# Optimization experiments

Hardware: AMD Instinct MI355X
Metric: run time of the kernel (lower is better)

The kernel has to match this reference:

```python
import jax, jax.numpy as jnp
import numpy as np

# dims (Nemotron-H 8B class mamba mixer)
HID = 4096      # hidden_size
NH = 128        # mamba_num_heads
HD = 64         # mamba_head_dim
DIN = NH * HD   # intermediate_size = 8192
G = 8           # n_groups
N = 128         # ssm_state_size
K = 4           # conv_kernel
CS = 256        # chunk_size
EPS = 1e-5
GROUP_SIZE = DIN // G
CONV_DIM = DIN + 2 * G * N           # 10240
PROJ = DIN + CONV_DIM + NH           # 18560 = gate | xBC | dt


def segment_sum(x):
    """x: [..., k] -> [..., k, k]; out[i,j] = sum_{m=j+1..i} x[m], -inf above diag."""
    k = x.shape[-1]
    xe = jnp.broadcast_to(x[..., None], x.shape + (k,))
    xe = jnp.where(jnp.tril(jnp.ones((k, k), bool), -1), xe, 0.0)
    s = jnp.cumsum(xe, axis=-2)
    return jnp.where(jnp.tril(jnp.ones((k, k), bool), 0), s, -jnp.inf)


def setup_inputs() -> dict:
    key = jax.random.key(0)
    ks = jax.random.split(key, 9)
    std = 0.02
    return {
        "hidden_states": jax.random.normal(ks[0], (2, 2048, HID), jnp.float32),
        "in_proj_w": jax.random.normal(ks[1], (PROJ, HID), jnp.float32) * std,
        "conv_w": jax.random.normal(ks[2], (CONV_DIM, 1, K), jnp.float32) * 0.1,
        "conv_b": jax.random.normal(ks[3], (CONV_DIM,), jnp.float32) * 0.01,
        "dt_bias": jax.random.uniform(ks[4], (NH,), jnp.float32, -4.0, -2.0),
        "A_log": jnp.log(jax.random.uniform(ks[5], (NH,), jnp.float32, 1.0, 16.0)),
        "D": jnp.ones((NH,), jnp.float32),
        "norm_w": jnp.ones((DIN,), jnp.float32),
        "out_proj_w": jax.random.normal(ks[8], (HID, DIN), jnp.float32) * std,
    }


def reference(hidden_states, in_proj_w, conv_w, conv_b, dt_bias, A_log, D, norm_w, out_proj_w):
    b, l, _ = hidden_states.shape
    zxbcdt = hidden_states @ in_proj_w.T                       # [b,l,PROJ]
    gate = zxbcdt[..., :DIN]
    xBC = zxbcdt[..., DIN:DIN + CONV_DIM]
    dt = zxbcdt[..., DIN + CONV_DIM:]                          # [b,l,NH]

    # causal depthwise conv1d + silu
    conv = jax.lax.conv_general_dilated(
        jnp.transpose(xBC, (0, 2, 1)), conv_w, (1,), [(K - 1, 0)],
        feature_group_count=CONV_DIM, dimension_numbers=("NCH", "OIH", "NCH"))
    xBC = jax.nn.silu(jnp.transpose(conv + conv_b[None, :, None], (0, 2, 1)))

    x = xBC[..., :DIN].reshape(b, l, NH, HD)
    B = xBC[..., DIN:DIN + G * N].reshape(b, l, G, N)
    C = xBC[..., DIN + G * N:].reshape(b, l, G, N)
    B = jnp.repeat(B, NH // G, axis=2)                         # [b,l,NH,N]
    C = jnp.repeat(C, NH // G, axis=2)

    A = -jnp.exp(A_log)                                        # [NH]
    dt = jax.nn.softplus(dt + dt_bias)                         # [b,l,NH]; limit (0,inf) is a no-op

    pad = (CS - l % CS) % CS
    def padl(t):
        return jnp.pad(t, [(0, 0), (0, pad)] + [(0, 0)] * (t.ndim - 2))

    D_res = D[None, None, :, None] * padl(x)                   # [b,L,NH,HD]
    xs = x * dt[..., None]
    Adt = A[None, None, :] * dt                                # [b,l,NH]

    nc = (l + pad) // CS
    def chunk(t):
        return padl(t).reshape((b, nc, CS) + t.shape[2:])
    xs, B, C = chunk(xs), chunk(B), chunk(C)                   # [b,c,k,h,*]
    Ac = jnp.transpose(chunk(Adt), (0, 3, 1, 2))               # [b,h,c,k]
    A_cumsum = jnp.cumsum(Ac, axis=-1)

    # 1. intra-chunk (diagonal blocks)
    L = jnp.exp(segment_sum(Ac))                               # [b,h,c,k,k]
    Gm = jnp.einsum("bcihn,bcjhn->bhcij", C, B)
    Y_diag = jnp.einsum("bhcij,bcjhd->bcihd", Gm * L, xs)

    # 2. chunk states
    decay_states = jnp.exp(A_cumsum[..., -1:] - A_cumsum)      # [b,h,c,k]
    states = jnp.einsum("bckhn,bhck,bckhd->bchdn", B, decay_states, xs)

    # 3. inter-chunk recurrence
    A_tail = jnp.pad(A_cumsum[..., -1], ((0, 0), (0, 0), (1, 0)))
    decay_chunk = jnp.exp(segment_sum(A_tail))                 # [b,h,c+1,c+1]
    states = jnp.concatenate([jnp.zeros_like(states[:, :1]), states], axis=1)
    new_states = jnp.einsum("bhzc,bchdn->bzhdn", decay_chunk, states)
    states = new_states[:, :-1]                                # [b,c,h,d,n]

    # 4. state -> output
    state_decay = jnp.exp(A_cumsum)                            # [b,h,c,k]
    Y_off = jnp.einsum("bckhn,bchdn,bhck->bckhd", C, states, state_decay)

    y = (Y_diag + Y_off).reshape(b, l + pad, NH, HD) + D_res
    y = y[:, :l].reshape(b, l, DIN)

    # gated grouped RMSNorm
    y = y * jax.nn.silu(gate)
    yg = y.reshape(b, l, G, GROUP_SIZE)
    var = jnp.mean(yg * yg, axis=-1, keepdims=True)
    y = (yg * jax.lax.rsqrt(var + EPS)).reshape(b, l, DIN) * norm_w
    return y @ out_proj_w.T
```

## Files before the change

### kernel.cpp

```cpp
#include <hip/hip_runtime.h>
#include <hip/hip_bf16.h>
#include <math.h>

#define HID 4096
#define NH 128
#define HD 64
#define DIN 8192
#define G 8
#define NSTATE 128
#define CS 256
#define GROUP_SIZE 1024
#define CONV_DIM 10240
#define ZXW 18432
#define BATCH 2
#define SEQ 2048
#define NT (BATCH*SEQ)
#define NC 8
#define DTSK 16

typedef __attribute__((ext_vector_type(8))) short bf16x8;
typedef __attribute__((ext_vector_type(4))) float f32x4;
typedef __attribute__((ext_vector_type(8))) unsigned short u16x8;
typedef __attribute__((ext_vector_type(4))) unsigned short u16x4;

__device__ __forceinline__ float sigmoidf_(float x){ return 1.f/(1.f+expf(-x)); }
__device__ __forceinline__ float siluf_(float x){ return x*sigmoidf_(x); }
__device__ __forceinline__ float softplusf_(float x){ return (x>20.f)? x : log1pf(expf(x)); }
__device__ __forceinline__ float b2f(unsigned short u){ union{unsigned int i; float f;} x; x.i = ((unsigned int)u)<<16; return x.f; }
__device__ __forceinline__ unsigned short f2b(float f){ __hip_bfloat16 h = __float2bfloat16(f); return *(unsigned short*)&h; }

__device__ __forceinline__ void gload_lds16(const void* g, void* l) {
  __builtin_amdgcn_global_load_lds((const __attribute__((address_space(1))) unsigned int*)g,
                                   (__attribute__((address_space(3))) unsigned int*)l, 16, 0, 0);
}
__device__ __forceinline__ bf16x8 ld8bf(const __hip_bfloat16* p){ return *(const bf16x8*)p; }

__device__ __forceinline__ void cast8(const float* in, __hip_bfloat16* out) {
  const float4* p = (const float4*)in;
  float4 a = p[0], b = p[1];
  union { __hip_bfloat16 h[8]; int4 v; } o;
  o.h[0]=__float2bfloat16(a.x); o.h[1]=__float2bfloat16(a.y);
  o.h[2]=__float2bfloat16(a.z); o.h[3]=__float2bfloat16(a.w);
  o.h[4]=__float2bfloat16(b.x); o.h[5]=__float2bfloat16(b.y);
  o.h[6]=__float2bfloat16(b.z); o.h[7]=__float2bfloat16(b.w);
  *(int4*)out = o.v;
}

__global__ __launch_bounds__(256)
void cast3_kernel(const float* __restrict__ hs, __hip_bfloat16* __restrict__ hs_bf,
                  const float* __restrict__ w_in, __hip_bfloat16* __restrict__ w_in_bf,
                  const float* __restrict__ w_out, __hip_bfloat16* __restrict__ w_out_bf) {
  const size_t n0 = (size_t)NT*HID/8;
  const size_t n1 = (size_t)ZXW*HID/8;
  const size_t n2 = (size_t)HID*DIN/8;
  const size_t ntot = n0 + n1 + n2;
  size_t i = (size_t)blockIdx.x * 256 + threadIdx.x;
  size_t stride = (size_t)gridDim.x * 256;
  for (; i < ntot; i += stride) {
    if (i < n0)            cast8(hs   + i*8,        hs_bf   + i*8);
    else if (i < n0 + n1)  cast8(w_in + (i-n0)*8,   w_in_bf + (i-n0)*8);
    else                   cast8(w_out+ (i-n0-n1)*8, w_out_bf+ (i-n0-n1)*8);
  }
}

template<bool OUT_BF16>
__global__ __launch_bounds__(512)
void gemm_bf16_256(const __hip_bfloat16* __restrict__ A, const __hip_bfloat16* __restrict__ B,
                   void* __restrict__ Cout, int M, int N, int K) {
  const int nMt = M >> 8, nNt = N >> 8;
  const int nwg = nMt * nNt;
  const int cpx = nwg >> 3;
  const int lin = blockIdx.x;
  const int swz = (lin & 7) * cpx + (lin >> 3);
  const int mt = swz % nMt, ntile = swz / nMt;
  const int rowBase = mt << 8;
  const int colBase = ntile << 8;

  __shared__ short As[4][8192];
  __shared__ short Bs[4][8192];

  const int tid = threadIdx.x;
  const int lane = tid & 63, wid = tid >> 6;
  const int wr = wid >> 2, wc = wid & 3;
  const int l15 = lane & 15, l4 = lane >> 4;

  const int r0 = tid >> 2,        c0 = (tid & 3) ^ ((r0 >> 1) & 3);
  const int r1 = (512+tid) >> 2,  c1 = ((512+tid) & 3) ^ ((r1 >> 1) & 3);
  const __hip_bfloat16* gA0 = A + (size_t)(rowBase + r0)*K + c0*8;
  const __hip_bfloat16* gA1 = A + (size_t)(rowBase + r1)*K + c1*8;
  const __hip_bfloat16* gB0 = B + (size_t)(colBase + r0)*K + c0*8;
  const __hip_bfloat16* gB1 = B + (size_t)(colBase + r1)*K + c1*8;
  const int ld0 = wid*512, ld1 = 4096 + wid*512;

#define STAGE_A(q, kt) do { \
    gload_lds16(gA0 + (size_t)(kt)*32, (void*)&As[q][ld0]); \
    gload_lds16(gA1 + (size_t)(kt)*32, (void*)&As[q][ld1]); \
  } while(0)
#define STAGE_B(q, kt) do { \
    gload_lds16(gB0 + (size_t)(kt)*32, (void*)&Bs[q][ld0]); \
    gload_lds16(gB1 + (size_t)(kt)*32, (void*)&Bs[q][ld1]); \
  } while(0)

  int aoff[8], boff[4];
  #pragma unroll
  for (int m=0;m<8;++m){ int r = wr*128 + m*16 + l15; aoff[m] = r*32 + ((l4 ^ ((r>>1)&3))*8); }
  #pragma unroll
  for (int n=0;n<4;++n){ int r = wc*64  + n*16 + l15; boff[n] = r*32 + ((l4 ^ ((r>>1)&3))*8); }

  f32x4 acc[8][4] = {};
  const int NKT = K >> 5;

  STAGE_A(0,0); STAGE_B(0,0);
  STAGE_A(1,1); STAGE_B(1,1);
  STAGE_A(2,2); STAGE_B(2,2);
  asm volatile("s_waitcnt vmcnt(8)" ::: "memory");
  __builtin_amdgcn_s_barrier();

  for (int t = 0; t < NKT; ++t) {
    const short* ab = &As[t&3][0];
    const short* bb = &Bs[t&3][0];
    const int q3 = (t+3)&3;
    bf16x8 a[4], b[4], a2[4];
    #pragma unroll
    for (int m=0;m<4;++m) a[m] = *(const bf16x8*)&ab[aoff[m]];
    #pragma unroll
    for (int n=0;n<4;++n) b[n] = *(const bf16x8*)&bb[boff[n]];
    if (t + 3 < NKT) STAGE_A(q3, t+3);
    __builtin_amdgcn_s_barrier();
    asm volatile("s_waitcnt lgkmcnt(0)" ::: "memory");
    __builtin_amdgcn_sched_barrier(0);
    __builtin_amdgcn_s_setprio(1);
    #pragma unroll
    for (int m=0;m<4;++m)
      #pragma unroll
      for (int n=0;n<4;++n)
        acc[m][n] = __builtin_amdgcn_mfma_f32_16x16x32_bf16(a[m], b[n], acc[m][n], 0, 0, 0);
    __builtin_amdgcn_s_setprio(0);
    __builtin_amdgcn_s_barrier();
    #pragma unroll
    for (int m=0;m<4;++m) a2[m] = *(const bf16x8*)&ab[aoff[m+4]];
    if (t + 3 < NKT) STAGE_B(q3, t+3);
    const int rem = NKT - 1 - t;
    if (rem >= 3)      asm volatile("s_waitcnt vmcnt(8)" ::: "memory");
    else if (rem == 2) asm volatile("s_waitcnt vmcnt(4)" ::: "memory");
    else if (rem == 1) asm volatile("s_waitcnt vmcnt(0)" ::: "memory");
    __builtin_amdgcn_s_barrier();
    asm volatile("s_waitcnt lgkmcnt(0)" ::: "memory");
    __builtin_amdgcn_sched_barrier(0);
    __builtin_amdgcn_s_setprio(1);
    #pragma unroll
    for (int m=0;m<4;++m)
      #pragma unroll
      for (int n=0;n<4;++n)
        acc[m+4][n] = __builtin_amdgcn_mfma_f32_16x16x32_bf16(a2[m], b[n], acc[m+4][n], 0, 0, 0);
    __builtin_amdgcn_s_setprio(0);
    __builtin_amdgcn_s_barrier();
  }
#undef STAGE_A
#undef STAGE_B

  #pragma unroll
  for (int m=0;m<8;++m) {
    int row0 = rowBase + wr*128 + m*16 + l4*4;
    #pragma unroll
    for (int n=0;n<4;++n) {
      int col = colBase + wc*64 + n*16 + l15;
      #pragma unroll
      for (int j=0;j<4;++j) {
        if (OUT_BF16)
          ((__hip_bfloat16*)Cout)[(size_t)(row0+j)*N + col] = __float2bfloat16(acc[m][n][j]);
        else
          ((float*)Cout)[(size_t)(row0+j)*N + col] = acc[m][n][j];
      }
    }
  }
}

__global__ __launch_bounds__(256)
void dt_gemm_splitk(const float* __restrict__ A, const float* __restrict__ B,
                    float* __restrict__ partial) {
  __shared__ float As[16][132];
  __shared__ float Bs[16][132];
  const int tid = threadIdx.x;
  const int tx = tid & 15, ty = tid >> 4;
  const int rowBase = blockIdx.y * 128;
  const int k0 = blockIdx.x * (HID/DTSK);
  float acc[8][8] = {};
  for (int kt = k0; kt < k0 + HID/DTSK; kt += 16) {
    for (int e = tid; e < 128*16; e += 256) {
      int r = e >> 4, c = e & 15;
      As[c][r] = A[(size_t)(rowBase + r) * HID + kt + c];
      Bs[c][r] = B[(size_t)r * HID + kt + c];
    }
    __syncthreads();
    #pragma unroll
    for (int kk = 0; kk < 16; ++kk) {
      float a[8], bv[8];
      #pragma unroll
      for (int i = 0; i < 8; ++i) a[i] = As[kk][ty*8+i];
      #pragma unroll
      for (int j = 0; j < 8; ++j) bv[j] = Bs[kk][tx*8+j];
      #pragma unroll
      for (int i = 0; i < 8; ++i)
        #pragma unroll
        for (int j = 0; j < 8; ++j)
          acc[i][j] += a[i]*bv[j];
    }
    __syncthreads();
  }
  float* outp = partial + (size_t)blockIdx.x * NT * NH;
  for (int i = 0; i < 8; ++i) {
    size_t ro = (size_t)(rowBase + ty*8 + i) * NH + tx*8;
    #pragma unroll
    for (int j = 0; j < 8; ++j) outp[ro + j] = acc[i][j];
  }
}

__global__ __launch_bounds__(256)
void dt_scan_kernel(const float* __restrict__ partial, const float* __restrict__ dt_bias,
                    const float* __restrict__ A_log, float* __restrict__ dt_sp,
                    float* __restrict__ Acs) {
  int bid = blockIdx.x;
  int c = bid % NC;
  int h = (bid / NC) % NH;
  int b = bid / (NC*NH);
  int k = threadIdx.x;
  int t = b*SEQ + c*CS + k;
  float raw = dt_bias[h];
  #pragma unroll
  for (int sk = 0; sk < DTSK; ++sk) raw += partial[(size_t)sk*NT*NH + (size_t)t*NH + h];
  float dtv = softplusf_(raw);
  dt_sp[(size_t)t*NH + h] = dtv;
  float adt = -expf(A_log[h]) * dtv;
  __shared__ float s[CS];
  s[k] = adt;
  __syncthreads();
  for (int off = 1; off < CS; off <<= 1) {
    float v = (k >= off) ? s[k-off] : 0.f;
    __syncthreads();
    s[k] += v;
    __syncthreads();
  }
  Acs[((size_t)(b*NH + h)*NC + c)*CS + k] = s[k];
}

__global__ __launch_bounds__(256)
void conv_fused_kernel(const __hip_bfloat16* __restrict__ zx, const float* __restrict__ w,
                       const float* __restrict__ bias,
                       const float* __restrict__ dt_sp, const float* __restrict__ Acs,
                       __hip_bfloat16* __restrict__ xsT, __hip_bfloat16* __restrict__ xwT,
                       __hip_bfloat16* __restrict__ Bbf, __hip_bfloat16* __restrict__ Cbf,
                       __hip_bfloat16* __restrict__ BT) {
  const int tt = blockIdx.x;
  const int ct = blockIdx.y;
  const int t0 = tt*64;
  const int ch0 = ct*64;
  const int tid = threadIdx.x;
  __shared__ unsigned short T[64][72];
  __shared__ float dts[64], ews[64];

  const bool isX = (ch0 < DIN);
  const bool isB = (ch0 >= DIN) && (ch0 < DIN + G*NSTATE);

  if (isX && tid < 64) {
    int h = ch0 >> 6;
    int t = t0 + tid;
    dts[tid] = dt_sp[(size_t)t*NH + h];
    int b = t0 >> 11, cc = (t0 >> 8) & 7, k0 = t0 & 255;
    const float* acs = Acs + ((size_t)(b*NH+h)*NC + cc)*CS;
    ews[tid] = __expf(acs[CS-1] - acs[k0 + tid]);
  }

  const int l0 = t0 & (SEQ-1);
  #pragma unroll
  for (int it = 0; it < 2; ++it) {
    int r = tid >> 2;
    int c8 = (tid & 3) + it*4;
    int cb = ch0 + c8*8;
    float acc[8];
    *(float4*)&acc[0] = *(const float4*)&bias[cb];
    *(float4*)&acc[4] = *(const float4*)&bias[cb+4];
    float4 wv[8];
    #pragma unroll
    for (int q=0;q<8;++q) wv[q] = *(const float4*)&w[(cb+q)*4];
    #pragma unroll
    for (int k=0;k<4;++k) {
      if (l0 + r - 3 + k >= 0) {
        u16x8 v = *(const u16x8*)&zx[(size_t)(t0+r-3+k)*ZXW + DIN + cb];
        #pragma unroll
        for (int q=0;q<8;++q) acc[q] += b2f(v[q]) * ((const float*)&wv[q])[k];
      }
    }
    u16x8 o;
    #pragma unroll
    for (int q=0;q<8;++q) o[q] = f2b(siluf_(acc[q]));
    if (isX || isB) {
      #pragma unroll
      for (int q=0;q<8;++q) T[c8*8+q][r] = o[q];
    }
    if (!isX) {
      if (isB) *(u16x8*)&Bbf[(size_t)(t0+r)*(G*NSTATE) + (cb - DIN)] = o;
      else     *(u16x8*)&Cbf[(size_t)(t0+r)*(G*NSTATE) + (cb - DIN - G*NSTATE)] = o;
    }
  }
  if (!isX && !isB) return;
  __syncthreads();
  #pragma unroll
  for (int it = 0; it < 2; ++it) {
    int ch = tid >> 2;
    int tc = (tid & 3) + it*4;
    u16x8 v = *(const u16x8*)&T[ch][tc*8];
    if (isX) {
      u16x8 a, wv2;
      #pragma unroll
      for (int q=0;q<8;++q) {
        float f = b2f(v[q]);
        float fs = f * dts[tc*8+q];
        a[q]   = f2b(fs);
        wv2[q] = f2b(fs * ews[tc*8+q]);
      }
      *(u16x8*)&xsT[(size_t)(ch0+ch)*NT + t0 + tc*8] = a;
      *(u16x8*)&xwT[(size_t)(ch0+ch)*NT + t0 + tc*8] = wv2;
    } else {
      *(u16x8*)&BT[(size_t)(ch0 - DIN + ch)*NT + t0 + tc*8] = v;
    }
  }
}

__global__ __launch_bounds__(256)
void chunk_states_mfma(const __hip_bfloat16* __restrict__ xwT, const __hip_bfloat16* __restrict__ BT,
                       float* __restrict__ states) {
  int h = blockIdx.x, bc = blockIdx.y;
  int g = h >> 4;
  int b = bc >> 3, c = bc & 7;
  int tbase = b*SEQ + c*CS;
  int tid = threadIdx.x, lane = tid & 63, w = tid >> 6;
  int l15 = lane & 15, l4 = lane >> 4;
  int n0 = w*32;
  const __hip_bfloat16* xp = xwT + (size_t)(h*64 + l15)*NT + tbase + l4*8;
  const __hip_bfloat16* bp = BT + (size_t)(g*128 + n0 + l15)*NT + tbase + l4*8;
  f32x4 acc[4][2] = {};
  for (int kc = 0; kc < 8; ++kc) {
    bf16x8 xf[4], bf2[2];
    #pragma unroll
    for (int tm=0;tm<4;++tm) xf[tm] = ld8bf(xp + (size_t)(tm*16)*NT + kc*32);
    #pragma unroll
    for (int tn=0;tn<2;++tn) bf2[tn] = ld8bf(bp + (size_t)(tn*16)*NT + kc*32);
    #pragma unroll
    for (int tm=0;tm<4;++tm)
      #pragma unroll
      for (int tn=0;tn<2;++tn)
        acc[tm][tn] = __builtin_amdgcn_mfma_f32_16x16x32_bf16(xf[tm], bf2[tn], acc[tm][tn], 0, 0, 0);
  }
  float* out = states + ((size_t)bc*NH + h)*(HD*NSTATE);
  #pragma unroll
  for (int tm=0;tm<4;++tm)
    #pragma unroll
    for (int tn=0;tn<2;++tn)
      #pragma unroll
      for (int q=0;q<4;++q)
        out[(size_t)(tm*16 + l4*4 + q)*NSTATE + n0 + tn*16 + l15] = acc[tm][tn][q];
}

__global__ void state_recurrence_kernel(const float* __restrict__ states, const float* __restrict__ Acs,
                                        __hip_bfloat16* __restrict__ states_bf) {
  int idx = blockIdx.x*256 + threadIdx.x;
  int dn = idx & 8191;
  int h = (idx >> 13) & 127;
  int b = idx >> 20;
  float S = 0.f;
  for (int c = 0; c < NC; ++c) {
    size_t off = ((size_t)(b*NC + c)*NH + h)*8192 + dn;
    float v = states[off];
    states_bf[off] = __float2bfloat16(S);
    float decay = expf(Acs[((size_t)(b*NH+h)*NC + c)*CS + CS-1]);
    S = S*decay + v;
  }
}

__global__ __launch_bounds__(256)
void y_mfma_kernel(const __hip_bfloat16* __restrict__ zx,
                   const __hip_bfloat16* __restrict__ Cn,
                   const __hip_bfloat16* __restrict__ Bn,
                   const __hip_bfloat16* __restrict__ xsT,
                   const __hip_bfloat16* __restrict__ Sbf,
                   const float* __restrict__ dt_sp,
                   const float* __restrict__ Acs,
                   const float* __restrict__ Dp,
                   __hip_bfloat16* __restrict__ ybf) {
  int h = blockIdx.x;
  int bc = blockIdx.y;
  int c = bc & 7, b = bc >> 3;
  int g = h >> 4;
  int tbase = b*SEQ + c*CS;
  int tid = threadIdx.x, lane = tid & 63, w = tid >> 6;
  int l15 = lane & 15, l4 = lane >> 4;
  int i0 = w*64;
  __shared__ float acs_s[CS];
  __shared__ unsigned short P[4][64][72];
  acs_s[tid] = Acs[((size_t)(b*NH+h)*NC + c)*CS + tid];
  __syncthreads();

  float acs_i[4], rd[4];
  float Dh = Dp[h];
  #pragma unroll
  for (int ti=0;ti<4;++ti) {
    int ig = i0 + ti*16 + l15;
    acs_i[ti] = acs_s[ig];
    rd[ti] = Dh / dt_sp[(size_t)(tbase+ig)*NH + h];
  }
  const __hip_bfloat16* Cbase = Cn + (size_t)tbase*1024 + g*128;
  const __hip_bfloat16* Bbase = Bn + (size_t)tbase*1024 + g*128;
  const __hip_bfloat16* xbase = xsT + (size_t)(h*64 + l15)*NT + tbase;

  f32x4 accY[4][4] = {};
  for (int jb = 0; jb <= w; ++jb) {
    int j0 = jb*64;
    f32x4 sacc[4][4] = {};
    for (int kc = 0; kc < 4; ++kc) {
      bf16x8 bfr[4], cfr[4];
      #pragma unroll
      for (int tj=0;tj<4;++tj) bfr[tj] = ld8bf(Bbase + (size_t)(j0 + tj*16 + l15)*1024 + kc*32 + l4*8);
      #pragma unroll
      for (int ti=0;ti<4;++ti) cfr[ti] = ld8bf(Cbase + (size_t)(i0 + ti*16 + l15)*1024 + kc*32 + l4*8);
      #pragma unroll
      for (int tj=0;tj<4;++tj)
        #pragma unroll
        for (int ti=0;ti<4;++ti)
          sacc[tj][ti] = __builtin_amdgcn_mfma_f32_16x16x32_bf16(bfr[tj], cfr[ti], sacc[tj][ti], 0, 0, 0);
    }
    #pragma unroll
    for (int tj=0;tj<4;++tj)
      #pragma unroll
      for (int ti=0;ti<4;++ti) {
        int ig = i0 + ti*16 + l15;
        float ai = acs_i[ti];
        u16x4 pk;
        #pragma unroll
        for (int q=0;q<4;++q) {
          int jg = j0 + tj*16 + l4*4 + q;
          float v = (jg <= ig) ? sacc[tj][ti][q] * __expf(ai - acs_s[jg]) : 0.f;
          if (jg == ig) v += rd[ti];
          pk[q] = f2b(v);
        }
        *(u16x4*)&P[w][ti*16 + l15][tj*16 + l4*4] = pk;
      }
    #pragma unroll
    for (int kc2 = 0; kc2 < 2; ++kc2) {
      bf16x8 xf[4], pf[4];
      #pragma unroll
      for (int tm=0;tm<4;++tm) xf[tm] = ld8bf(xbase + (size_t)(tm*16)*NT + j0 + kc2*32 + l4*8);
      #pragma unroll
      for (int ti=0;ti<4;++ti) pf[ti] = *(const bf16x8*)&P[w][ti*16 + l15][kc2*32 + l4*8];
      #pragma unroll
      for (int tm=0;tm<4;++tm)
        #pragma unroll
        for (int ti=0;ti<4;++ti)
          accY[tm][ti] = __builtin_amdgcn_mfma_f32_16x16x32_bf16(xf[tm], pf[ti], accY[tm][ti], 0, 0, 0);
    }
  }
  const __hip_bfloat16* Sb = Sbf + ((size_t)bc*NH + h)*(HD*NSTATE);
  f32x4 oacc[4][4] = {};
  for (int kc = 0; kc < 4; ++kc) {
    bf16x8 sf[4], cfr[4];
    #pragma unroll
    for (int tm=0;tm<4;++tm) sf[tm] = ld8bf(Sb + (size_t)(tm*16 + l15)*NSTATE + kc*32 + l4*8);
    #pragma unroll
    for (int ti=0;ti<4;++ti) cfr[ti] = ld8bf(Cbase + (size_t)(i0 + ti*16 + l15)*1024 + kc*32 + l4*8);
    #pragma unroll
    for (int tm=0;tm<4;++tm)
      #pragma unroll
      for (int ti=0;ti<4;++ti)
        oacc[tm][ti] = __builtin_amdgcn_mfma_f32_16x16x32_bf16(sf[tm], cfr[ti], oacc[tm][ti], 0, 0, 0);
  }
  #pragma unroll
  for (int ti=0;ti<4;++ti) {
    int ig = i0 + ti*16 + l15;
    int t = tbase + ig;
    float sd = __expf(acs_i[ti]);
    #pragma unroll
    for (int tm=0;tm<4;++tm) {
      int ch0 = h*64 + tm*16 + l4*4;
      u16x4 gv = *(const u16x4*)&zx[(size_t)t*ZXW + ch0];
      u16x4 out;
      #pragma unroll
      for (int q=0;q<4;++q) {
        float yv = accY[tm][ti][q] + sd * oacc[tm][ti][q];
        yv *= siluf_(b2f(gv[q]));
        out[q] = f2b(yv);
      }
      *(u16x4*)&ybf[(size_t)t*DIN + ch0] = out;
    }
  }
}

__global__ __launch_bounds__(256)
void groupnorm_bf16_kernel(unsigned short* __restrict__ y, const float* __restrict__ norm_w) {
  int bid = blockIdx.x;
  int g = bid % G;
  int t = bid / G;
  unsigned short* yp = y + (size_t)t*DIN + g*GROUP_SIZE;
  int tid = threadIdx.x;
  u16x4 v = *(const u16x4*)&yp[tid*4];
  float f[4]; float ss = 0.f;
  #pragma unroll
  for (int j=0;j<4;++j) { f[j] = b2f(v[j]); ss += f[j]*f[j]; }
  #pragma unroll
  for (int off = 32; off > 0; off >>= 1) ss += __shfl_xor(ss, off);
  __shared__ float wsum[4];
  int wave = tid >> 6;
  if ((tid & 63) == 0) wsum[wave] = ss;
  __syncthreads();
  float tot = wsum[0]+wsum[1]+wsum[2]+wsum[3];
  float rs = rsqrtf(tot/(float)GROUP_SIZE + 1e-5f);
  const float* nw = norm_w + g*GROUP_SIZE + tid*4;
  u16x4 o;
  #pragma unroll
  for (int j=0;j<4;++j) o[j] = f2b(f[j] * rs * nw[j]);
  *(u16x4*)&yp[tid*4] = o;
}

extern "C" void kernel_launch(void* const* d_in, const int* in_sizes, int n_in,
                              void* d_out, int out_size, void* d_ws, size_t ws_size,
                              hipStream_t stream) {
  const float* hs        = (const float*)d_in[0];
  const float* in_proj_w = (const float*)d_in[1];
  const float* conv_w    = (const float*)d_in[2];
  const float* conv_b    = (const float*)d_in[3];
  const float* dt_bias   = (const float*)d_in[4];
  const float* A_log     = (const float*)d_in[5];
  const float* Dp        = (const float*)d_in[6];
  const float* norm_w    = (const float*)d_in[7];
  const float* out_proj_w= (const float*)d_in[8];
  float* outp = (float*)d_out;

  char* ws = (char*)d_ws;
  __hip_bfloat16* zx_bf = (__hip_bfloat16*)ws;
  char* p = ws + (size_t)NT*ZXW*2;
  __hip_bfloat16* B_bf  = (__hip_bfloat16*)p; p += (size_t)NT*G*NSTATE*2;
  __hip_bfloat16* C_bf  = (__hip_bfloat16*)p; p += (size_t)NT*G*NSTATE*2;
  __hip_bfloat16* BT    = (__hip_bfloat16*)p; p += (size_t)NT*G*NSTATE*2;
  float* states = (float*)p;  p += (size_t)BATCH*NC*NH*HD*NSTATE*4;
  __hip_bfloat16* y_bf  = (__hip_bfloat16*)p; p += (size_t)NT*DIN*2;
  float* dtb    = (float*)p;  p += (size_t)NT*NH*4;
  float* Acs    = (float*)p;  p += (size_t)BATCH*NH*NC*CS*4;
  float* dt_part = (float*)y_bf;
  char* F = p;
  __hip_bfloat16* w_in_bf   = (__hip_bfloat16*)F;
  __hip_bfloat16* xsT       = (__hip_bfloat16*)F;
  __hip_bfloat16* xwT       = (__hip_bfloat16*)(F + 67108864);
  __hip_bfloat16* hs_bf     = (__hip_bfloat16*)(F + 150994944);
  __hip_bfloat16* states_bf = (__hip_bfloat16*)(F + 150994944);
  char* F2 = F + 150994944 + 33554432;
  __hip_bfloat16* w_out_bf  = (__hip_bfloat16*)F2;

  dt_gemm_splitk<<<dim3(DTSK, NT/128), 256, 0, stream>>>(hs, in_proj_w + (size_t)ZXW*HID, dt_part);
  dt_scan_kernel<<<BATCH*NH*NC, CS, 0, stream>>>(dt_part, dt_bias, A_log, dtb, Acs);

  cast3_kernel<<<4096, 256, 0, stream>>>(hs, hs_bf, in_proj_w, w_in_bf, out_proj_w, w_out_bf);

  gemm_bf16_256<true><<<dim3((NT/256)*(ZXW/256)), 512, 0, stream>>>(
      hs_bf, w_in_bf, zx_bf, NT, ZXW, HID);

  conv_fused_kernel<<<dim3(NT/64, CONV_DIM/64), 256, 0, stream>>>(
      zx_bf, conv_w, conv_b, dtb, Acs, xsT, xwT, B_bf, C_bf, BT);

  chunk_states_mfma<<<dim3(NH, BATCH*NC), 256, 0, stream>>>(xwT, BT, states);
  state_recurrence_kernel<<<(BATCH*NH*HD*NSTATE)/256, 256, 0, stream>>>(states, Acs, states_bf);
  y_mfma_kernel<<<dim3(NH, BATCH*NC), 256, 0, stream>>>(zx_bf, C_bf, B_bf, xsT, states_bf, dtb, Acs, Dp, y_bf);
  groupnorm_bf16_kernel<<<NT*G, 256, 0, stream>>>((unsigned short*)y_bf, norm_w);

  gemm_bf16_256<false><<<dim3((NT/256)*(HID/256)), 512, 0, stream>>>(
      y_bf, w_out_bf, outp, NT, HID, DIN);
}
```

Baseline: 1.816 ms.

## Fuse chunk-state GEMM with inter-chunk recurrence and hidden-state cast into dt GEMM

```diff
diff --git a/kernel.cpp b/kernel.cpp
--- a/kernel.cpp
+++ b/kernel.cpp
@@ -47,19 +47,16 @@
 }
 
 __global__ __launch_bounds__(256)
-void cast3_kernel(const float* __restrict__ hs, __hip_bfloat16* __restrict__ hs_bf,
-                  const float* __restrict__ w_in, __hip_bfloat16* __restrict__ w_in_bf,
+void cast2_kernel(const float* __restrict__ w_in, __hip_bfloat16* __restrict__ w_in_bf,
                   const float* __restrict__ w_out, __hip_bfloat16* __restrict__ w_out_bf) {
-  const size_t n0 = (size_t)NT*HID/8;
   const size_t n1 = (size_t)ZXW*HID/8;
   const size_t n2 = (size_t)HID*DIN/8;
-  const size_t ntot = n0 + n1 + n2;
+  const size_t ntot = n1 + n2;
   size_t i = (size_t)blockIdx.x * 256 + threadIdx.x;
   size_t stride = (size_t)gridDim.x * 256;
   for (; i < ntot; i += stride) {
-    if (i < n0)            cast8(hs   + i*8,        hs_bf   + i*8);
-    else if (i < n0 + n1)  cast8(w_in + (i-n0)*8,   w_in_bf + (i-n0)*8);
-    else                   cast8(w_out+ (i-n0-n1)*8, w_out_bf+ (i-n0-n1)*8);
+    if (i < n1)  cast8(w_in + i*8,      w_in_bf + i*8);
+    else         cast8(w_out+ (i-n1)*8, w_out_bf+ (i-n1)*8);
   }
 }
 
@@ -178,7 +175,7 @@
 
 __global__ __launch_bounds__(256)
 void dt_gemm_splitk(const float* __restrict__ A, const float* __restrict__ B,
-                    float* __restrict__ partial) {
+                    float* __restrict__ partial, __hip_bfloat16* __restrict__ hs_bf) {
   __shared__ float As[16][132];
   __shared__ float Bs[16][132];
   const int tid = threadIdx.x;
@@ -189,7 +186,9 @@
   for (int kt = k0; kt < k0 + HID/DTSK; kt += 16) {
     for (int e = tid; e < 128*16; e += 256) {
       int r = e >> 4, c = e & 15;
-      As[c][r] = A[(size_t)(rowBase + r) * HID + kt + c];
+      float av = A[(size_t)(rowBase + r) * HID + kt + c];
+      As[c][r] = av;
+      hs_bf[(size_t)(rowBase + r) * HID + kt + c] = __float2bfloat16(av);
       Bs[c][r] = B[(size_t)r * HID + kt + c];
     }
     __syncthreads();
@@ -328,53 +327,42 @@
 }
 
 __global__ __launch_bounds__(256)
-void chunk_states_mfma(const __hip_bfloat16* __restrict__ xwT, const __hip_bfloat16* __restrict__ BT,
-                       float* __restrict__ states) {
-  int h = blockIdx.x, bc = blockIdx.y;
+void chunk_states_fused(const __hip_bfloat16* __restrict__ xwT, const __hip_bfloat16* __restrict__ BT,
+                        const float* __restrict__ Acs, __hip_bfloat16* __restrict__ states_bf) {
+  int h = blockIdx.x, b = blockIdx.y;
   int g = h >> 4;
-  int b = bc >> 3, c = bc & 7;
-  int tbase = b*SEQ + c*CS;
   int tid = threadIdx.x, lane = tid & 63, w = tid >> 6;
   int l15 = lane & 15, l4 = lane >> 4;
   int n0 = w*32;
-  const __hip_bfloat16* xp = xwT + (size_t)(h*64 + l15)*NT + tbase + l4*8;
-  const __hip_bfloat16* bp = BT + (size_t)(g*128 + n0 + l15)*NT + tbase + l4*8;
-  f32x4 acc[4][2] = {};
-  for (int kc = 0; kc < 8; ++kc) {
-    bf16x8 xf[4], bf2[2];
-    #pragma unroll
-    for (int tm=0;tm<4;++tm) xf[tm] = ld8bf(xp + (size_t)(tm*16)*NT + kc*32);
-    #pragma unroll
-    for (int tn=0;tn<2;++tn) bf2[tn] = ld8bf(bp + (size_t)(tn*16)*NT + kc*32);
+  f32x4 S[4][2] = {};
+  for (int c = 0; c < NC; ++c) {
+    int tbase = b*SEQ + c*CS;
+    const __hip_bfloat16* xp = xwT + (size_t)(h*64 + l15)*NT + tbase + l4*8;
+    const __hip_bfloat16* bp = BT + (size_t)(g*128 + n0 + l15)*NT + tbase + l4*8;
+    f32x4 acc[4][2] = {};
+    for (int kc = 0; kc < 8; ++kc) {
+      bf16x8 xf[4], bf2[2];
+      #pragma unroll
+      for (int tm=0;tm<4;++tm) xf[tm] = ld8bf(xp + (size_t)(tm*16)*NT + kc*32);
+      #pragma unroll
+      for (int tn=0;tn<2;++tn) bf2[tn] = ld8bf(bp + (size_t)(tn*16)*NT + kc*32);
+      #pragma unroll
+      for (int tm=0;tm<4;++tm)
+        #pragma unroll
+        for (int tn=0;tn<2;++tn)
+          acc[tm][tn] = __builtin_amdgcn_mfma_f32_16x16x32_bf16(xf[tm], bf2[tn], acc[tm][tn], 0, 0, 0);
+    }
+    __hip_bfloat16* out = states_bf + ((size_t)(b*NC + c)*NH + h)*(HD*NSTATE);
+    float decay = expf(Acs[((size_t)(b*NH+h)*NC + c)*CS + CS-1]);
     #pragma unroll
     for (int tm=0;tm<4;++tm)
       #pragma unroll
       for (int tn=0;tn<2;++tn)
-        acc[tm][tn] = __builtin_amdgcn_mfma_f32_16x16x32_bf16(xf[tm], bf2[tn], acc[tm][tn], 0, 0, 0);
-  }
-  float* out = states + ((size_t)bc*NH + h)*(HD*NSTATE);
-  #pragma unroll
-  for (int tm=0;tm<4;++tm)
-    #pragma unroll
-    for (int tn=0;tn<2;++tn)
-      #pragma unroll
-      for (int q=0;q<4;++q)
-        out[(size_t)(tm*16 + l4*4 + q)*NSTATE + n0 + tn*16 + l15] = acc[tm][tn][q];
-}
-
-__global__ void state_recurrence_kernel(const float* __restrict__ states, const float* __restrict__ Acs,
-                                        __hip_bfloat16* __restrict__ states_bf) {
-  int idx = blockIdx.x*256 + threadIdx.x;
-  int dn = idx & 8191;
-  int h = (idx >> 13) & 127;
-  int b = idx >> 20;
-  float S = 0.f;
-  for (int c = 0; c < NC; ++c) {
-    size_t off = ((size_t)(b*NC + c)*NH + h)*8192 + dn;
-    float v = states[off];
-    states_bf[off] = __float2bfloat16(S);
-    float decay = expf(Acs[((size_t)(b*NH+h)*NC + c)*CS + CS-1]);
-    S = S*decay + v;
+        #pragma unroll
+        for (int q=0;q<4;++q) {
+          out[(size_t)(tm*16 + l4*4 + q)*NSTATE + n0 + tn*16 + l15] = __float2bfloat16(S[tm][tn][q]);
+          S[tm][tn][q] = S[tm][tn][q]*decay + acc[tm][tn][q];
+        }
   }
 }
 
@@ -540,7 +528,6 @@
   __hip_bfloat16* B_bf  = (__hip_bfloat16*)p; p += (size_t)NT*G*NSTATE*2;
   __hip_bfloat16* C_bf  = (__hip_bfloat16*)p; p += (size_t)NT*G*NSTATE*2;
   __hip_bfloat16* BT    = (__hip_bfloat16*)p; p += (size_t)NT*G*NSTATE*2;
-  float* states = (float*)p;  p += (size_t)BATCH*NC*NH*HD*NSTATE*4;
   __hip_bfloat16* y_bf  = (__hip_bfloat16*)p; p += (size_t)NT*DIN*2;
   float* dtb    = (float*)p;  p += (size_t)NT*NH*4;
   float* Acs    = (float*)p;  p += (size_t)BATCH*NH*NC*CS*4;
@@ -554,10 +541,10 @@
   char* F2 = F + 150994944 + 33554432;
   __hip_bfloat16* w_out_bf  = (__hip_bfloat16*)F2;
 
-  dt_gemm_splitk<<<dim3(DTSK, NT/128), 256, 0, stream>>>(hs, in_proj_w + (size_t)ZXW*HID, dt_part);
+  dt_gemm_splitk<<<dim3(DTSK, NT/128), 256, 0, stream>>>(hs, in_proj_w + (size_t)ZXW*HID, dt_part, hs_bf);
   dt_scan_kernel<<<BATCH*NH*NC, CS, 0, stream>>>(dt_part, dt_bias, A_log, dtb, Acs);
 
-  cast3_kernel<<<4096, 256, 0, stream>>>(hs, hs_bf, in_proj_w, w_in_bf, out_proj_w, w_out_bf);
+  cast2_kernel<<<4096, 256, 0, stream>>>(in_proj_w, w_in_bf, out_proj_w, w_out_bf);
 
   gemm_bf16_256<true><<<dim3((NT/256)*(ZXW/256)), 512, 0, stream>>>(
       hs_bf, w_in_bf, zx_bf, NT, ZXW, HID);
@@ -565,8 +552,8 @@
   conv_fused_kernel<<<dim3(NT/64, CONV_DIM/64), 256, 0, stream>>>(
       zx_bf, conv_w, conv_b, dtb, Acs, xsT, xwT, B_bf, C_bf, BT);
 
-  chunk_states_mfma<<<dim3(NH, BATCH*NC), 256, 0, stream>>>(xwT, BT, states);
-  state_recurrence_kernel<<<(BATCH*NH*HD*NSTATE)/256, 256, 0, stream>>>(states, Acs, states_bf);
+  chunk_states_fused<<<dim3(NH, BATCH), 256, 0, stream>>>(xwT, BT, Acs, states_bf);
+
   y_mfma_kernel<<<dim3(NH, BATCH*NC), 256, 0, stream>>>(zx_bf, C_bf, B_bf, xsT, states_bf, dtb, Acs, Dp, y_bf);
   groupnorm_bf16_kernel<<<NT*G, 256, 0, stream>>>((unsigned short*)y_bf, norm_w);
 
```

Result: no change. 1.798 ms (-0.9%).
